# Optimization experiments

Hardware: AMD Instinct MI355X
Metric: run time of the kernel (lower is better)

Reference implementation:

```python
import jax, jax.numpy as jnp
import numpy as np

DIM = 192
NUM_HEADS = 8
EPS = 1e-12  # F.normalize default eps


def setup_inputs() -> dict:
    key = jax.random.key(0)
    ks = jax.random.split(key, 6)
    b, c, h, w = 8, DIM, 128, 128
    scale = 1.0 / np.sqrt(DIM)  # conv2d default init scale (approx)
    return {
        "input": jax.random.normal(ks[0], (b, c, h, w), dtype=jnp.float32),
        "color": jax.random.normal(ks[1], (b, c, h, w), dtype=jnp.float32),
        "Wq": jax.random.normal(ks[2], (DIM, DIM), dtype=jnp.float32) * scale,
        "Wk": jax.random.normal(ks[3], (DIM, DIM), dtype=jnp.float32) * scale,
        "Wv": jax.random.normal(ks[4], (DIM, DIM), dtype=jnp.float32) * scale,
        "Wo": jax.random.normal(ks[5], (DIM, DIM), dtype=jnp.float32) * scale,
    }


def _proj(x, W):
    # 1x1 conv (bias=False) == channel GEMM: [b,c,h,w] x [out,c] -> [b,out,h,w]
    return jnp.einsum('bchw,oc->bohw', x, W)


def _l2norm(x):
    n = jnp.sqrt(jnp.sum(x * x, axis=-1, keepdims=True))
    return x / jnp.maximum(n, EPS)


def reference(input, color, Wq, Wk, Wv, Wo):
    b, c, h, w = input.shape
    head = NUM_HEADS
    dh = c // head
    hw = h * w
    # q from color, k/v from input
    q = _proj(color, Wq).reshape(b, head, dh, hw)
    k = _proj(input, Wk).reshape(b, head, dh, hw)
    v = _proj(input, Wv).reshape(b, head, dh, hw)
    q = _l2norm(q)
    k = _l2norm(k)
    # transposed (channel) attention: [b,head,dh,dh]
    attn = jnp.einsum('bhcn,bhdn->bhcd', q, k)
    attn = jax.nn.softmax(attn, axis=-1)
    out = jnp.einsum('bhcd,bhdn->bhcn', attn, v)  # [b,head,dh,hw]
    out = out.reshape(b, c, h, w)
    return _proj(out, Wo)
```

## Files before the change

### kernel.cpp

```cpp
#include <hip/hip_runtime.h>
#include <hip/hip_bf16.h>


typedef __attribute__((ext_vector_type(4))) float f32x4;
typedef __attribute__((ext_vector_type(8))) short short8;

#define MFMA16(a, b, c) __builtin_amdgcn_mfma_f32_16x16x32_bf16((a), (b), (c), 0, 0, 0)

__device__ __forceinline__ unsigned int pack_rne(float a, float b) {
  unsigned int ua = __float_as_uint(a), ub = __float_as_uint(b);
  ua += 0x7fffu + ((ua >> 16) & 1u);
  ub += 0x7fffu + ((ub >> 16) & 1u);
  return (ua >> 16) | (ub & 0xffff0000u);
}
__device__ __forceinline__ unsigned short bf16u_rne(float x) {
  unsigned int u = __float_as_uint(x);
  u += 0x7fffu + ((u >> 16) & 1u);
  return (unsigned short)(u >> 16);
}
union S8U { short8 s; unsigned int u[4]; };
__device__ __forceinline__ short8 load_cvt8(const float* p) {
  f32x4 x = *(const f32x4*)p;
  f32x4 y = *(const f32x4*)(p + 4);
  S8U r;
  r.u[0] = pack_rne(x[0], x[1]);
  r.u[1] = pack_rne(x[2], x[3]);
  r.u[2] = pack_rne(y[0], y[1]);
  r.u[3] = pack_rne(y[2], y[3]);
  return r.s;
}

#define HW 16384
#define CDIM 192
#define NB 8
#define GSZ (CDIM * CDIM)
#define NTILE 300
#define FSLOT 24576
#define BROW 80

__global__ void k0_wvt(const float* __restrict__ Wv, unsigned short* __restrict__ WvT) {
  int idx = blockIdx.x * 256 + threadIdx.x;
  if (idx < CDIM * CDIM) {
    int j = idx / CDIM, cp = idx % CDIM;
    WvT[idx] = bf16u_rne(Wv[(size_t)cp * CDIM + j]);
  }
}

__device__ __forceinline__ short8 bfrag(const char* buf, int row, int lg) {
  return *(const short8*)(buf + row * BROW + lg * 16);
}

__device__ __forceinline__ void stageC(const float* __restrict__ ib,
                                       const float* __restrict__ cb, int col0,
                                       char* fdst, int wave, int lane) {
#pragma unroll
  for (int i = 0; i < 2; ++i) {
    const int g = wave * 2 + i;
    const int tensor = g >= 12;
    const int row = (g - (tensor ? 12 : 0)) * 16 + (lane >> 2);
    const float* T = tensor ? cb : ib;
    const float* gp = T + (size_t)row * HW + col0 + (lane & 3) * 4;
    __builtin_amdgcn_global_load_lds(
        (const __attribute__((address_space(1))) void*)gp,
        (__attribute__((address_space(3))) void*)(fdst + g * 1024), 16, 0, 0);
  }
}

template <int W>
__device__ __forceinline__ void pair_step(const char* bb, f32x4 (&acc)[25],
                                          int l15, int lg) {
  const short8 aT = bfrag(bb, W * 16 + l15, lg);
  const short8 aB = bfrag(bb, (23 - W) * 16 + l15, lg);
#pragma unroll
  for (int ct = W; ct < 24; ++ct) {
    const short8 b = bfrag(bb, ct * 16 + l15, lg);
    acc[ct - W] = MFMA16(aT, b, acc[ct - W]);
    if (ct >= 23 - W) acc[ct + 1] = MFMA16(aB, b, acc[ct + 1]);
  }
}

__device__ __forceinline__ void pair_dispatch(int wave, const char* bb,
                                              f32x4 (&acc)[25], int l15, int lg) {
  switch (wave) {
    case 0: pair_step<0>(bb, acc, l15, lg); break;
    case 1: pair_step<1>(bb, acc, l15, lg); break;
    case 2: pair_step<2>(bb, acc, l15, lg); break;
    case 3: pair_step<3>(bb, acc, l15, lg); break;
    case 4: pair_step<4>(bb, acc, l15, lg); break;
    case 5: pair_step<5>(bb, acc, l15, lg); break;
    case 6: pair_step<6>(bb, acc, l15, lg); break;
    case 7: pair_step<7>(bb, acc, l15, lg); break;
    case 8: pair_step<8>(bb, acc, l15, lg); break;
    case 9: pair_step<9>(bb, acc, l15, lg); break;
    case 10: pair_step<10>(bb, acc, l15, lg); break;
    default: pair_step<11>(bb, acc, l15, lg); break;
  }
}

__global__ __launch_bounds__(768) void gram2_k(const float* __restrict__ input,
                                               const float* __restrict__ color,
                                               float* __restrict__ part,
                                               int npart, int ncp) {
  __shared__ __align__(16) char fbuf[4][FSLOT];
  __shared__ __align__(16) char bbuf[384 * BROW];
  const int tid = threadIdx.x, wave = tid >> 6, lane = tid & 63;
  const int l15 = lane & 15, lg = (lane >> 4) & 3;
  const int strip = blockIdx.x, b = blockIdx.y;
  const float* ib = input + (size_t)b * CDIM * HW;
  const float* cb = color + (size_t)b * CDIM * HW;
  const int ch0 = strip * ncp * 2;

  f32x4 acc[25];
#pragma unroll
  for (int i = 0; i < 25; ++i) acc[i] = (f32x4){0.f, 0.f, 0.f, 0.f};

  stageC(ib, cb, (ch0 + 0) * 16, fbuf[0], wave, lane);
  stageC(ib, cb, (ch0 + 1) * 16, fbuf[1], wave, lane);
  stageC(ib, cb, (ch0 + 2) * 16, fbuf[2], wave, lane);
  stageC(ib, cb, (ch0 + 3) * 16, fbuf[3], wave, lane);

#pragma unroll 1
  for (int cp = 0; cp < ncp; ++cp) {
    if (cp + 1 < ncp) {
      asm volatile("s_waitcnt vmcnt(4)" ::: "memory");
    } else {
      asm volatile("s_waitcnt vmcnt(0)" ::: "memory");
    }
    __builtin_amdgcn_sched_barrier(0);
    __builtin_amdgcn_s_barrier();
    {
      const char* sA = fbuf[(2 * cp) & 3];
      const char* sB = fbuf[(2 * cp + 1) & 3];
#pragma unroll
      for (int u0 = 0; u0 < 2; ++u0) {
        const int u = tid + u0 * 768;
        const int zr = u >> 2, sub = u & 3;
        const char* src = (sub < 2 ? sA : sB) + zr * 64 + (sub & 1) * 32;
        f32x4 x = *(const f32x4*)src;
        f32x4 y = *(const f32x4*)(src + 16);
        S8U pk;
        pk.u[0] = pack_rne(x[0], x[1]);
        pk.u[1] = pack_rne(x[2], x[3]);
        pk.u[2] = pack_rne(y[0], y[1]);
        pk.u[3] = pack_rne(y[2], y[3]);
        *(short8*)(bbuf + zr * BROW + sub * 16) = pk.s;
      }
    }
    asm volatile("s_waitcnt lgkmcnt(0)" ::: "memory");
    __builtin_amdgcn_sched_barrier(0);
    __builtin_amdgcn_s_barrier();
    if (cp + 2 < ncp) {
      stageC(ib, cb, (ch0 + 2 * cp + 4) * 16, fbuf[(2 * cp + 4) & 3], wave, lane);
      stageC(ib, cb, (ch0 + 2 * cp + 5) * 16, fbuf[(2 * cp + 5) & 3], wave, lane);
    }
    pair_dispatch(wave, bbuf, acc, l15, lg);
  }

  float* pbase = part + (size_t)(b * npart + strip) * NTILE * 256;
#pragma unroll
  for (int s = 0; s < 25; ++s)
    *(f32x4*)(pbase + ((size_t)(wave * 25 + s) * 64 + lane) * 4) = acc[s];
}

template <int NP>
__global__ __launch_bounds__(256) void reduce_k(const float* __restrict__ part,
                                                float* __restrict__ G) {
  const int b = blockIdx.y;
  const int T = blockIdx.x * 4 + (threadIdx.x >> 6);
  const int lane = threadIdx.x & 63;
  const float* p = part + ((size_t)b * NP * NTILE + T) * 256 + lane * 4;
  f32x4 v[NP];
#pragma unroll
  for (int s = 0; s < NP; ++s) v[s] = *(const f32x4*)(p + (size_t)s * NTILE * 256);
  f32x4 sum = v[0];
#pragma unroll
  for (int s = 1; s < NP; ++s) {
    sum[0] += v[s][0]; sum[1] += v[s][1]; sum[2] += v[s][2]; sum[3] += v[s][3];
  }
  const int w = T / 25, s = T % 25;
  int rt, ct;
  if (s <= 23 - w) { rt = w; ct = w + s; }
  else { rt = 23 - w; ct = s - 1; }
  int type, gm, gn;
  if (ct < 12) { type = 2; gm = rt; gn = ct; }
  else if (rt < 12) { type = 0; gm = rt; gn = ct - 12; }
  else { type = 1; gm = rt - 12; gn = ct - 12; }
  float* Gm = G + ((size_t)type * NB + b) * GSZ;
  const int l15 = lane & 15, lg = lane >> 4;
  const int row0 = gm * 16 + lg * 4, col = gn * 16 + l15;
#pragma unroll
  for (int r = 0; r < 4; ++r) Gm[(size_t)(row0 + r) * CDIM + col] = sum[r];
  if (type != 0 && rt != ct) {
#pragma unroll
    for (int r = 0; r < 4; ++r) Gm[(size_t)col * CDIM + (row0 + r)] = sum[r];
  }
}

__global__ __launch_bounds__(256) void k2a(const float* __restrict__ G,
                                           const float* __restrict__ Wq,
                                           const float* __restrict__ Wk,
                                           float* __restrict__ A_pre,
                                           float* __restrict__ nqk) {
  const int b = blockIdx.x, type = blockIdx.y;
  __shared__ __align__(16) unsigned short Hs[192][200];
  const int tid = threadIdx.x, wave = tid >> 6, lane = tid & 63;
  const int l15 = lane & 15, lg = lane >> 4, row0 = wave * 48;
  const float* W1 = (type == 2) ? Wk : Wq;
  const float* Gm = G + ((size_t)type * NB + b) * GSZ;

  f32x4 acc[3][12];
#pragma unroll
  for (int t = 0; t < 3; t++)
#pragma unroll
    for (int j = 0; j < 12; j++) acc[t][j] = (f32x4){0.f, 0.f, 0.f, 0.f};

  for (int ks = 0; ks < 192; ks += 32) {
    short8 afr[3];
#pragma unroll
    for (int t = 0; t < 3; t++)
      afr[t] = load_cvt8(W1 + (size_t)(row0 + t * 16 + l15) * CDIM + ks + lg * 8);
#pragma unroll
    for (int tj = 0; tj < 12; tj++) {
      short8 bfr = load_cvt8(Gm + (size_t)(tj * 16 + l15) * CDIM + ks + lg * 8);
#pragma unroll
      for (int t = 0; t < 3; t++) acc[t][tj] = MFMA16(afr[t], bfr, acc[t][tj]);
    }
  }
#pragma unroll
  for (int t = 0; t < 3; t++)
#pragma unroll
    for (int tj = 0; tj < 12; tj++)
#pragma unroll
      for (int r = 0; r < 4; r++)
        Hs[row0 + t * 16 + lg * 4 + r][tj * 16 + l15] = bf16u_rne(acc[t][tj][r]);
  __syncthreads();

  if (type == 0) {
    f32x4 a2[3][12];
#pragma unroll
    for (int t = 0; t < 3; t++)
#pragma unroll
      for (int j = 0; j < 12; j++) a2[t][j] = (f32x4){0.f, 0.f, 0.f, 0.f};
    for (int ks = 0; ks < 192; ks += 32) {
      short8 afr[3];
#pragma unroll
      for (int t = 0; t < 3; t++)
        afr[t] = *(const short8*)&Hs[row0 + t * 16 + l15][ks + lg * 8];
#pragma unroll
      for (int tj = 0; tj < 12; tj++) {
        short8 bfr = load_cvt8(Wk + (size_t)(tj * 16 + l15) * CDIM + ks + lg * 8);
#pragma unroll
        for (int t = 0; t < 3; t++) a2[t][tj] = MFMA16(afr[t], bfr, a2[t][tj]);
      }
    }
    float* Ab = A_pre + (size_t)b * GSZ;
#pragma unroll
    for (int t = 0; t < 3; t++)
#pragma unroll
      for (int tj = 0; tj < 12; tj++)
#pragma unroll
        for (int r = 0; r < 4; r++)
          Ab[(size_t)(row0 + t * 16 + lg * 4 + r) * CDIM + tj * 16 + l15] = a2[t][tj][r];
  } else {
    f32x4 a2[3];
#pragma unroll
    for (int t = 0; t < 3; t++) a2[t] = (f32x4){0.f, 0.f, 0.f, 0.f};
    for (int ks = 0; ks < 192; ks += 32) {
#pragma unroll
      for (int t = 0; t < 3; t++) {
        short8 afr = *(const short8*)&Hs[row0 + t * 16 + l15][ks + lg * 8];
        short8 bfr = load_cvt8(W1 + (size_t)(row0 + t * 16 + l15) * CDIM + ks + lg * 8);
        a2[t] = MFMA16(afr, bfr, a2[t]);
      }
    }
    float* dst = nqk + ((size_t)(type - 1) * NB + b) * CDIM;
#pragma unroll
    for (int t = 0; t < 3; t++)
#pragma unroll
      for (int r = 0; r < 4; r++)
        if (lg * 4 + r == l15) dst[row0 + t * 16 + l15] = a2[t][r];
  }
}

__global__ void k2b(const float* __restrict__ A_pre, const float* __restrict__ nqk,
                    float* __restrict__ attnw) {
  const int b = blockIdx.x, tid = threadIdx.x;
  const int h = tid >> 5, r = tid & 31;
  if (r >= 24) return;
  const float* Ab = A_pre + (size_t)b * GSZ;
  const float* nq = nqk + (size_t)b * CDIM;
  const float* nk = nqk + (size_t)(NB + b) * CDIM;
  const int c = h * 24 + r;
  const float qn = rsqrtf(fmaxf(nq[c], 1e-24f));
  float e[24];
  float mx = -1e30f;
#pragma unroll
  for (int d = 0; d < 24; d++) {
    float kn = rsqrtf(fmaxf(nk[h * 24 + d], 1e-24f));
    float l = Ab[(size_t)c * CDIM + h * 24 + d] * qn * kn;
    e[d] = l;
    mx = fmaxf(mx, l);
  }
  float s = 0.f;
#pragma unroll
  for (int d = 0; d < 24; d++) {
    float x = __expf(e[d] - mx);
    e[d] = x;
    s += x;
  }
  const float inv = 1.0f / s;
  float* dst = attnw + (((size_t)b * NB + h) * 24 + r) * 24;
#pragma unroll
  for (int d = 0; d < 24; d++) dst[d] = e[d] * inv;
}

__global__ __launch_bounds__(256) void k3(const float* __restrict__ attnw,
                                          const float* __restrict__ Wo,
                                          const unsigned short* __restrict__ WvT,
                                          unsigned short* __restrict__ Pbf) {
  const int b = blockIdx.x;
  __shared__ __align__(16) unsigned short AT[192][200];
  __shared__ __align__(16) unsigned short Ms[192][200];
  const int tid = threadIdx.x, wave = tid >> 6, lane = tid & 63;
  const int l15 = lane & 15, lg = lane >> 4, row0 = wave * 48;

  unsigned int* ATu = (unsigned int*)&AT[0][0];
  for (int i = tid; i < 192 * 100; i += 256) ATu[i] = 0u;
  __syncthreads();
  const float* at = attnw + (size_t)b * NB * 24 * 24;
  for (int i = tid; i < 4608; i += 256) {
    int h = i / 576, rem = i % 576, c = rem / 24, d = rem % 24;
    AT[h * 24 + d][h * 24 + c] = bf16u_rne(at[(h * 24 + c) * 24 + d]);
  }
  __syncthreads();

  f32x4 acc[3][12];
#pragma unroll
  for (int t = 0; t < 3; t++)
#pragma unroll
    for (int j = 0; j < 12; j++) acc[t][j] = (f32x4){0.f, 0.f, 0.f, 0.f};
  for (int ks = 0; ks < 192; ks += 32) {
    short8 afr[3];
#pragma unroll
    for (int t = 0; t < 3; t++)
      afr[t] = load_cvt8(Wo + (size_t)(row0 + t * 16 + l15) * CDIM + ks + lg * 8);
#pragma unroll
    for (int tj = 0; tj < 12; tj++) {
      short8 bfr = *(const short8*)&AT[tj * 16 + l15][ks + lg * 8];
#pragma unroll
      for (int t = 0; t < 3; t++) acc[t][tj] = MFMA16(afr[t], bfr, acc[t][tj]);
    }
  }
#pragma unroll
  for (int t = 0; t < 3; t++)
#pragma unroll
    for (int tj = 0; tj < 12; tj++)
#pragma unroll
      for (int r = 0; r < 4; r++)
        Ms[row0 + t * 16 + lg * 4 + r][tj * 16 + l15] = bf16u_rne(acc[t][tj][r]);
  __syncthreads();

  f32x4 a2[3][12];
#pragma unroll
  for (int t = 0; t < 3; t++)
#pragma unroll
    for (int j = 0; j < 12; j++) a2[t][j] = (f32x4){0.f, 0.f, 0.f, 0.f};
  for (int ks = 0; ks < 192; ks += 32) {
    short8 afr[3];
#pragma unroll
    for (int t = 0; t < 3; t++)
      afr[t] = *(const short8*)&Ms[row0 + t * 16 + l15][ks + lg * 8];
#pragma unroll
    for (int tj = 0; tj < 12; tj++) {
      short8 bfr = *(const short8*)(WvT + (size_t)(tj * 16 + l15) * CDIM + ks + lg * 8);
#pragma unroll
      for (int t = 0; t < 3; t++) a2[t][tj] = MFMA16(afr[t], bfr, a2[t][tj]);
    }
  }
  unsigned short* Pb = Pbf + (size_t)b * GSZ;
#pragma unroll
  for (int t = 0; t < 3; t++)
#pragma unroll
    for (int tj = 0; tj < 12; tj++)
#pragma unroll
      for (int r = 0; r < 4; r++)
        Pb[(size_t)(row0 + t * 16 + lg * 4 + r) * CDIM + tj * 16 + l15] = bf16u_rne(a2[t][tj][r]);
}

__global__ __launch_bounds__(256) void kD(const unsigned short* __restrict__ Pbf,
                                          const float* __restrict__ input,
                                          float* __restrict__ out) {
  const int nchunk = blockIdx.x, b = blockIdx.y;
  const int n0 = nchunk * 128;
  __shared__ __align__(16) char BsT[128 * 384];
  const int tid = threadIdx.x, wave = tid >> 6, lane = tid & 63;
  const int l15 = lane & 15, lg = lane >> 4, row0 = wave * 48;

  {
    const int n4 = (tid & 31) * 4;
    const int kb0 = (tid >> 5) * 4;
    const float* src = input + (size_t)b * CDIM * HW + n0 + n4;
    f32x4 w[24];
#pragma unroll
    for (int rnd = 0; rnd < 6; ++rnd)
#pragma unroll
      for (int j = 0; j < 4; ++j)
        w[rnd * 4 + j] = *(const f32x4*)(src + (size_t)(kb0 + rnd * 32 + j) * HW);
    __builtin_amdgcn_sched_barrier(0);
    char* bsb = BsT;
#pragma unroll
    for (int rnd = 0; rnd < 6; ++rnd) {
      const int kb = kb0 + rnd * 32;
#pragma unroll
      for (int i = 0; i < 4; ++i) {
        const int n = n4 + i;
        unsigned long long pk =
            (unsigned long long)pack_rne(w[rnd * 4 + 0][i], w[rnd * 4 + 1][i]) |
            ((unsigned long long)pack_rne(w[rnd * 4 + 2][i], w[rnd * 4 + 3][i]) << 32);
        *(unsigned long long*)(bsb + n * 384 + ((kb * 2) ^ ((n & 7) << 4))) = pk;
      }
    }
  }
  __syncthreads();

  f32x4 acc[3][8];
#pragma unroll
  for (int t = 0; t < 3; t++)
#pragma unroll
    for (int j = 0; j < 8; j++) acc[t][j] = (f32x4){0.f, 0.f, 0.f, 0.f};

  const unsigned short* Pb = Pbf + (size_t)b * GSZ;
#pragma unroll 2
  for (int ks = 0; ks < 6; ks++) {
    short8 afr[3];
#pragma unroll
    for (int t = 0; t < 3; t++)
      afr[t] = *(const short8*)(Pb + (size_t)(row0 + t * 16 + l15) * CDIM + ks * 32 + lg * 8);
#pragma unroll
    for (int tn = 0; tn < 8; tn++) {
      const int n = tn * 16 + l15;
      short8 bfr = *(const short8*)(BsT + n * 384 + ((ks * 64 + lg * 16) ^ ((n & 7) << 4)));
#pragma unroll
      for (int t = 0; t < 3; t++) acc[t][tn] = MFMA16(afr[t], bfr, acc[t][tn]);
    }
  }
  float* ob = out + (size_t)b * CDIM * HW + n0;
#pragma unroll
  for (int t = 0; t < 3; t++)
#pragma unroll
    for (int tn = 0; tn < 8; tn++)
#pragma unroll
      for (int r = 0; r < 4; r++) {
        const int m = row0 + t * 16 + lg * 4 + r;
        ob[(size_t)m * HW + tn * 16 + l15] = acc[t][tn][r];
      }
}

extern "C" void kernel_launch(void* const* d_in, const int* in_sizes, int n_in,
                              void* d_out, int out_size, void* d_ws, size_t ws_size,
                              hipStream_t stream) {
  const float* input = (const float*)d_in[0];
  const float* color = (const float*)d_in[1];
  const float* Wq = (const float*)d_in[2];
  const float* Wk = (const float*)d_in[3];
  const float* Wv = (const float*)d_in[4];
  const float* Wo = (const float*)d_in[5];
  float* out = (float*)d_out;
  char* ws = (char*)d_ws;

  const size_t OFF_G = 0;
  const size_t OFF_APRE = 3538944;
  const size_t OFF_NQK = OFF_APRE + 1179648;
  const size_t OFF_ATT = OFF_NQK + 12288;
  const size_t OFF_WVT = OFF_ATT + 147456;
  const size_t OFF_PBF = OFF_WVT + 73728;
  const size_t OFF_PART = OFF_PBF + 589824;

  float* G = (float*)(ws + OFF_G);
  float* A_pre = (float*)(ws + OFF_APRE);
  float* nqk = (float*)(ws + OFF_NQK);
  float* attnw = (float*)(ws + OFF_ATT);
  unsigned short* WvT = (unsigned short*)(ws + OFF_WVT);
  unsigned short* Pbf = (unsigned short*)(ws + OFF_PBF);
  float* part = (float*)(ws + OFF_PART);

  int npart = 32;
  while (npart > 2 && OFF_PART + (size_t)npart * NB * NTILE * 1024 > ws_size) npart >>= 1;
  const int ncp = 512 / npart;

  k0_wvt<<<dim3(144), dim3(256), 0, stream>>>(Wv, WvT);
  gram2_k<<<dim3(npart, NB), dim3(768), 0, stream>>>(input, color, part, npart, ncp);
  switch (npart) {
    case 32: reduce_k<32><<<dim3(75, NB), dim3(256), 0, stream>>>(part, G); break;
    case 16: reduce_k<16><<<dim3(75, NB), dim3(256), 0, stream>>>(part, G); break;
    case 8:  reduce_k<8><<<dim3(75, NB), dim3(256), 0, stream>>>(part, G); break;
    case 4:  reduce_k<4><<<dim3(75, NB), dim3(256), 0, stream>>>(part, G); break;
    default: reduce_k<2><<<dim3(75, NB), dim3(256), 0, stream>>>(part, G); break;
  }
  k2a<<<dim3(NB, 3), dim3(256), 0, stream>>>(G, Wq, Wk, A_pre, nqk);
  k2b<<<dim3(NB), dim3(256), 0, stream>>>(A_pre, nqk, attnw);
  k3<<<dim3(NB), dim3(256), 0, stream>>>(attnw, Wo, WvT, Pbf);
  kD<<<dim3(HW / 128, NB), dim3(256), 0, stream>>>(Pbf, input, out);
}
```

Before: 198.7 us.

## Split gram kernel into two 384-thread blocks per strip with double buffering

The Gram-matrix kernel now launches two 6-wave blocks per (strip, batch) instead of one 12-wave block. Each block computes half of the output tile pairs, selected by blockIdx.z, and three blocks may share a CU. The staging buffer drops from four slots to two and the explicit vmcnt waits are replaced by plain __syncthreads. This aims to raise occupancy and scheduling flexibility, but each block now loads and converts the full input strip, so global traffic doubles and loads no longer overlap with compute as deeply.

```diff
diff --git a/kernel.cpp b/kernel.cpp
--- a/kernel.cpp
+++ b/kernel.cpp
@@ -54,8 +54,8 @@
                                        const float* __restrict__ cb, int col0,
                                        char* fdst, int wave, int lane) {
 #pragma unroll
-  for (int i = 0; i < 2; ++i) {
-    const int g = wave * 2 + i;
+  for (int i = 0; i < 4; ++i) {
+    const int g = wave * 4 + i;
     const int tensor = g >= 12;
     const int row = (g - (tensor ? 12 : 0)) * 16 + (lane >> 2);
     const float* T = tensor ? cb : ib;
@@ -79,9 +79,9 @@
   }
 }
 
-__device__ __forceinline__ void pair_dispatch(int wave, const char* bb,
+__device__ __forceinline__ void pair_dispatch(int wp, const char* bb,
                                               f32x4 (&acc)[25], int l15, int lg) {
-  switch (wave) {
+  switch (wp) {
     case 0: pair_step<0>(bb, acc, l15, lg); break;
     case 1: pair_step<1>(bb, acc, l15, lg); break;
     case 2: pair_step<2>(bb, acc, l15, lg); break;
@@ -97,15 +97,16 @@
   }
 }
 
-__global__ __launch_bounds__(768) void gram2_k(const float* __restrict__ input,
-                                               const float* __restrict__ color,
-                                               float* __restrict__ part,
-                                               int npart, int ncp) {
-  __shared__ __align__(16) char fbuf[4][FSLOT];
+__global__ __launch_bounds__(384, 3) void gram2_k(const float* __restrict__ input,
+                                                  const float* __restrict__ color,
+                                                  float* __restrict__ part,
+                                                  int npart, int ncp) {
+  __shared__ __align__(16) char fbuf[2][FSLOT];
   __shared__ __align__(16) char bbuf[384 * BROW];
   const int tid = threadIdx.x, wave = tid >> 6, lane = tid & 63;
   const int l15 = lane & 15, lg = (lane >> 4) & 3;
-  const int strip = blockIdx.x, b = blockIdx.y;
+  const int strip = blockIdx.x, b = blockIdx.y, z = blockIdx.z;
+  const int wp = z * 6 + wave;
   const float* ib = input + (size_t)b * CDIM * HW;
   const float* cb = color + (size_t)b * CDIM * HW;
   const int ch0 = strip * ncp * 2;
@@ -116,24 +117,16 @@
 
   stageC(ib, cb, (ch0 + 0) * 16, fbuf[0], wave, lane);
   stageC(ib, cb, (ch0 + 1) * 16, fbuf[1], wave, lane);
-  stageC(ib, cb, (ch0 + 2) * 16, fbuf[2], wave, lane);
-  stageC(ib, cb, (ch0 + 3) * 16, fbuf[3], wave, lane);
 
 #pragma unroll 1
   for (int cp = 0; cp < ncp; ++cp) {
-    if (cp + 1 < ncp) {
-      asm volatile("s_waitcnt vmcnt(4)" ::: "memory");
-    } else {
-      asm volatile("s_waitcnt vmcnt(0)" ::: "memory");
-    }
-    __builtin_amdgcn_sched_barrier(0);
-    __builtin_amdgcn_s_barrier();
+    __syncthreads();
     {
-      const char* sA = fbuf[(2 * cp) & 3];
-      const char* sB = fbuf[(2 * cp + 1) & 3];
-#pragma unroll
-      for (int u0 = 0; u0 < 2; ++u0) {
-        const int u = tid + u0 * 768;
+      const char* sA = fbuf[0];
+      const char* sB = fbuf[1];
+#pragma unroll
+      for (int u0 = 0; u0 < 4; ++u0) {
+        const int u = tid + u0 * 384;
         const int zr = u >> 2, sub = u & 3;
         const char* src = (sub < 2 ? sA : sB) + zr * 64 + (sub & 1) * 32;
         f32x4 x = *(const f32x4*)src;
@@ -146,20 +139,18 @@
         *(short8*)(bbuf + zr * BROW + sub * 16) = pk.s;
       }
     }
-    asm volatile("s_waitcnt lgkmcnt(0)" ::: "memory");
-    __builtin_amdgcn_sched_barrier(0);
-    __builtin_amdgcn_s_barrier();
-    if (cp + 2 < ncp) {
-      stageC(ib, cb, (ch0 + 2 * cp + 4) * 16, fbuf[(2 * cp + 4) & 3], wave, lane);
-      stageC(ib, cb, (ch0 + 2 * cp + 5) * 16, fbuf[(2 * cp + 5) & 3], wave, lane);
-    }
-    pair_dispatch(wave, bbuf, acc, l15, lg);
+    __syncthreads();
+    if (cp + 1 < ncp) {
+      stageC(ib, cb, (ch0 + 2 * cp + 2) * 16, fbuf[0], wave, lane);
+      stageC(ib, cb, (ch0 + 2 * cp + 3) * 16, fbuf[1], wave, lane);
+    }
+    pair_dispatch(wp, bbuf, acc, l15, lg);
   }
 
   float* pbase = part + (size_t)(b * npart + strip) * NTILE * 256;
 #pragma unroll
   for (int s = 0; s < 25; ++s)
-    *(f32x4*)(pbase + ((size_t)(wave * 25 + s) * 64 + lane) * 4) = acc[s];
+    *(f32x4*)(pbase + ((size_t)(wp * 25 + s) * 64 + lane) * 4) = acc[s];
 }
 
 template <int NP>
@@ -489,7 +480,7 @@
   const int ncp = 512 / npart;
 
   k0_wvt<<<dim3(144), dim3(256), 0, stream>>>(Wv, WvT);
-  gram2_k<<<dim3(npart, NB), dim3(768), 0, stream>>>(input, color, part, npart, ncp);
+  gram2_k<<<dim3(npart, NB, 2), dim3(384), 0, stream>>>(input, color, part, npart, ncp);
   switch (npart) {
     case 32: reduce_k<32><<<dim3(75, NB), dim3(256), 0, stream>>>(part, G); break;
     case 16: reduce_k<16><<<dim3(75, NB), dim3(256), 0, stream>>>(part, G); break;
```

Result: slower. 713.7 us (+259.1%).
